# Performance work log

Measured on AMD Instinct MI355X. Metric: run time of the kernel, lower is better.

The kernel has to match this reference:

```python
import jax, jax.numpy as jnp
import numpy as np

FEATURE_DIM = 1024
N_HEADS = 16
D_K = 64
D_V = 64
B = 8
S = 1024
LN_EPS = 1e-5
NEG = 1e9


def setup_inputs() -> dict:
    key = jax.random.key(0)
    ks = jax.random.split(key, 7)
    sc = 0.02
    return {
        "input_Q": jax.random.normal(ks[0], (B, S, FEATURE_DIM), jnp.float32),
        "input_K": jax.random.normal(ks[1], (B, S, FEATURE_DIM), jnp.float32),
        "input_V": jax.random.normal(ks[2], (B, S, FEATURE_DIM), jnp.float32),
        "attn_mask": jnp.ones((B, S, S), jnp.float32),
        "W_Q": jax.random.normal(ks[3], (FEATURE_DIM, N_HEADS * D_K), jnp.float32) * sc,
        "W_K": jax.random.normal(ks[4], (FEATURE_DIM, N_HEADS * D_K), jnp.float32) * sc,
        "W_V": jax.random.normal(ks[5], (FEATURE_DIM, N_HEADS * D_V), jnp.float32) * sc,
        "W_O": jax.random.normal(ks[6], (N_HEADS * D_V, FEATURE_DIM), jnp.float32) * sc,
    }


def reference(input_Q, input_K, input_V, attn_mask, W_Q, W_K, W_V, W_O):
    b = input_Q.shape[0]
    # projections -> [b, h, s, d]
    Q = (input_Q @ W_Q).reshape(b, -1, N_HEADS, D_K).transpose(0, 2, 1, 3)
    K = (input_K @ W_K).reshape(b, -1, N_HEADS, D_K).transpose(0, 2, 1, 3)
    V = (input_V @ W_V).reshape(b, -1, N_HEADS, D_V).transpose(0, 2, 1, 3)
    # scores [b, h, sq, sk]
    scores = jnp.einsum("bhqd,bhkd->bhqk", Q, K) / np.sqrt(D_K).astype(np.float32)
    # additive mask: (mask - 1) * 1e9, broadcast over heads
    scores = scores + (attn_mask[:, None, :, :] - 1.0) * NEG
    attn = jax.nn.softmax(scores, axis=-1)
    # dropout is eval-mode identity (deterministic baseline)
    context = jnp.einsum("bhqk,bhkd->bhqd", attn, V)
    context = context.transpose(0, 2, 1, 3).reshape(b, -1, N_HEADS * D_V)
    output = context @ W_O
    x = output + input_Q  # residual
    # fresh nn.LayerNorm(feature_dim): weight=1, bias=0
    mu = jnp.mean(x, axis=-1, keepdims=True)
    var = jnp.var(x, axis=-1, keepdims=True)
    out = (x - mu) * jax.lax.rsqrt(var + LN_EPS)
    return out, attn
```

## Files before the change

kernel.cpp:

```cpp
#include <hip/hip_runtime.h>
#include <hip/hip_bf16.h>
#include <stdint.h>

typedef unsigned short u16;
typedef __attribute__((ext_vector_type(8))) short bf16x8;
typedef __attribute__((ext_vector_type(4))) float f32x4;

#define BATCH 8
#define SEQ   1024
#define FDIM  1024
#define NHEAD 16
#define DHEAD 64

__device__ __forceinline__ float bf2f(u16 u) {
  union { unsigned int i; float f; } v; v.i = ((unsigned int)u) << 16; return v.f;
}
__device__ __forceinline__ u16 f2bf(float f) {
  union { float f; unsigned int i; } v; v.f = f;
  unsigned int x = v.i;
  return (u16)((x + 0x7fffu + ((x >> 16) & 1u)) >> 16);
}

__device__ __forceinline__ uint4 load8(const u16* p) { return *(const uint4*)p; }
__device__ __forceinline__ uint4 load8(const float* p) {
  float4 a = *(const float4*)p;
  float4 b = *(const float4*)(p + 4);
  union { u16 h[8]; uint4 v; } r;
  r.h[0] = f2bf(a.x); r.h[1] = f2bf(a.y); r.h[2] = f2bf(a.z); r.h[3] = f2bf(a.w);
  r.h[4] = f2bf(b.x); r.h[5] = f2bf(b.y); r.h[6] = f2bf(b.z); r.h[7] = f2bf(b.w);
  return r.v;
}

__global__ __launch_bounds__(256) void transpose_k(
    const float* __restrict__ src, u16* __restrict__ dst, int srcLd, int dstLd) {
  __shared__ u16 t[64][72];
  const int r0 = blockIdx.y * 64, c0 = blockIdx.x * 64;
  const int tid = threadIdx.x;
  for (int p = 0; p < 16; ++p) {
    int idx = p * 256 + tid, r = idx >> 6, c = idx & 63;
    t[r][c] = f2bf(src[(long)(r0 + r) * srcLd + (c0 + c)]);
  }
  __syncthreads();
  for (int p = 0; p < 16; ++p) {
    int idx = p * 256 + tid, r = idx >> 6, c = idx & 63;
    dst[(long)(c0 + r) * dstLd + (r0 + c)] = t[c][r];
  }
}

template<int MODE, int WGM, int WGN, int MI, int NJ, typename AT>
__global__ __launch_bounds__(256) void gemm_bt(
    const AT* __restrict__ A, const u16* __restrict__ Bt, void* __restrict__ C,
    int K, int lda, int ldb, int ldc, long aZ, long bZ) {
  constexpr int BM = WGM * MI * 16;
  constexpr int BN = WGN * NJ * 16;
  __shared__ __align__(16) u16 As[BM][40];
  __shared__ __align__(16) u16 Bs[BN][40];
  const int tid = threadIdx.x;
  const int wave = tid >> 6, lane = tid & 63;
  const int quad = lane >> 4, l16 = lane & 15;
  const int wm = wave / WGN, wn = wave % WGN;
  const int m0 = blockIdx.y * BM, n0 = blockIdx.x * BN;
  const int z = blockIdx.z;
  A  += (long)z * aZ;
  Bt += (long)z * bZ;

  f32x4 acc[MI][NJ];
#pragma unroll
  for (int i = 0; i < MI; ++i)
#pragma unroll
    for (int j = 0; j < NJ; ++j) acc[i][j] = (f32x4){0.f, 0.f, 0.f, 0.f};

  const int srow = tid >> 2, scol = (tid & 3) * 8;
  for (int k0 = 0; k0 < K; k0 += 32) {
    __syncthreads();
#pragma unroll
    for (int p = 0; p < BM / 64; ++p) {
      int r = p * 64 + srow;
      *(uint4*)&As[r][scol] = load8(&A[(long)(m0 + r) * lda + k0 + scol]);
    }
#pragma unroll
    for (int p = 0; p < BN / 64; ++p) {
      int r = p * 64 + srow;
      *(uint4*)&Bs[r][scol] = load8(&Bt[(long)(n0 + r) * ldb + k0 + scol]);
    }
    __syncthreads();
    bf16x8 af[MI], bfr[NJ];
#pragma unroll
    for (int i = 0; i < MI; ++i)
      af[i] = *(const bf16x8*)&As[wm * MI * 16 + i * 16 + l16][quad * 8];
#pragma unroll
    for (int j = 0; j < NJ; ++j)
      bfr[j] = *(const bf16x8*)&Bs[wn * NJ * 16 + j * 16 + l16][quad * 8];
#pragma unroll
    for (int i = 0; i < MI; ++i)
#pragma unroll
      for (int j = 0; j < NJ; ++j)
        acc[i][j] = __builtin_amdgcn_mfma_f32_16x16x32_bf16(af[i], bfr[j], acc[i][j], 0, 0, 0);
  }

#pragma unroll
  for (int i = 0; i < MI; ++i) {
    const int rowb = m0 + wm * MI * 16 + i * 16 + quad * 4;
#pragma unroll
    for (int j = 0; j < NJ; ++j) {
      const int col = n0 + wn * NJ * 16 + j * 16 + l16;
#pragma unroll
      for (int r = 0; r < 4; ++r) {
        const float v = acc[i][j][r];
        const int row = rowb + r;
        if (MODE == 1) {
          ((float*)C)[(long)row * ldc + col] = v;
        } else if (MODE == 2) {
          int bb = row >> 10, ss = row & 1023, hh = col >> 6, dd = col & 63;
          ((u16*)C)[((long)(bb * NHEAD + hh) * SEQ + ss) * DHEAD + dd] = f2bf(v);
        } else if (MODE == 3) {
          int bb = row >> 10, ss = row & 1023, hh = col >> 6, dd = col & 63;
          ((u16*)C)[((long)(bb * NHEAD + hh) * DHEAD + dd) * SEQ + ss] = f2bf(v);
        } else {
          ((u16*)C)[(long)row * ldc + col] = f2bf(v);
        }
      }
    }
  }
}

__global__ __launch_bounds__(256, 4) void attn_kernel(
    const u16* __restrict__ Qb, const u16* __restrict__ Kb,
    const u16* __restrict__ Vt, const float* __restrict__ Msk,
    float* __restrict__ P, u16* __restrict__ Ctx) {
  __shared__ __align__(16) u16 QVs[64][72];
  __shared__ __align__(16) u16 Ks[64][72];
  __shared__ __align__(16) float Ps[64][68];
  const int tid = threadIdx.x, wave = tid >> 6, lane = tid & 63;
  const int quad = lane >> 4, l16 = lane & 15;
  const int q0 = blockIdx.x * 64, h = blockIdx.y, b = blockIdx.z;
  const long bh = (long)b * NHEAD + h;
  const u16* Qp = Qb + ((long)b * SEQ + q0) * FDIM + h * DHEAD;
  const u16* Kp = Kb + bh * SEQ * DHEAD;
  const u16* Vp = Vt + bh * (long)DHEAD * SEQ;
  const float* Mp = Msk + ((long)b * SEQ + q0) * SEQ;
  float* Pp = P + bh * (long)SEQ * SEQ + (long)q0 * SEQ;
  u16* Cp = Ctx + ((long)b * SEQ + q0) * FDIM + h * DHEAD;

  {
    int r = tid >> 3, c = (tid & 7) * 8;
    *(uint4*)&QVs[r][c]      = *(const uint4*)&Qp[(long)r * FDIM + c];
    *(uint4*)&QVs[r + 32][c] = *(const uint4*)&Qp[(long)(r + 32) * FDIM + c];
  }
  __syncthreads();
  const bf16x8 aq0 = *(const bf16x8*)&QVs[wave * 16 + l16][quad * 8];
  const bf16x8 aq1 = *(const bf16x8*)&QVs[wave * 16 + l16][32 + quad * 8];

  float m[4], l[4], rl[4];
#pragma unroll
  for (int r = 0; r < 4; ++r) { m[r] = -3.0e38f; l[r] = 0.f; }

  for (int st = 0; st < SEQ / 64; ++st) {
    const int sk0 = st * 64;
    __syncthreads();
    {
      int r = tid >> 3, c = (tid & 7) * 8;
      *(uint4*)&Ks[r][c]      = *(const uint4*)&Kp[(sk0 + r) * DHEAD + c];
      *(uint4*)&Ks[r + 32][c] = *(const uint4*)&Kp[(sk0 + r + 32) * DHEAD + c];
    }
    __syncthreads();
    float sv[4][4];
#pragma unroll
    for (int j = 0; j < 4; ++j) {
      bf16x8 bk0 = *(const bf16x8*)&Ks[j * 16 + l16][quad * 8];
      bf16x8 bk1 = *(const bf16x8*)&Ks[j * 16 + l16][32 + quad * 8];
      f32x4 sc = (f32x4){0.f, 0.f, 0.f, 0.f};
      sc = __builtin_amdgcn_mfma_f32_16x16x32_bf16(aq0, bk0, sc, 0, 0, 0);
      sc = __builtin_amdgcn_mfma_f32_16x16x32_bf16(aq1, bk1, sc, 0, 0, 0);
#pragma unroll
      for (int r = 0; r < 4; ++r) {
        int qr = wave * 16 + quad * 4 + r;
        float mk = Mp[(long)qr * SEQ + sk0 + j * 16 + l16];
        sv[j][r] = sc[r] * 0.125f + (mk - 1.0f) * 1.0e9f;
      }
    }
#pragma unroll
    for (int r = 0; r < 4; ++r) {
      float tm = fmaxf(fmaxf(sv[0][r], sv[1][r]), fmaxf(sv[2][r], sv[3][r]));
#pragma unroll
      for (int off = 1; off < 16; off <<= 1) tm = fmaxf(tm, __shfl_xor(tm, off, 64));
      float mn = fmaxf(m[r], tm);
      float ps = __expf(sv[0][r] - mn) + __expf(sv[1][r] - mn) +
                 __expf(sv[2][r] - mn) + __expf(sv[3][r] - mn);
#pragma unroll
      for (int off = 1; off < 16; off <<= 1) ps += __shfl_xor(ps, off, 64);
      l[r] = l[r] * __expf(m[r] - mn) + ps;
      m[r] = mn;
    }
  }
#pragma unroll
  for (int r = 0; r < 4; ++r) rl[r] = 1.0f / l[r];

  f32x4 acc[4];
#pragma unroll
  for (int n = 0; n < 4; ++n) acc[n] = (f32x4){0.f, 0.f, 0.f, 0.f};

  for (int st = 0; st < SEQ / 64; ++st) {
    const int sk0 = st * 64;
    __syncthreads();
    {
      int r = tid >> 3, c = (tid & 7) * 8;
      *(uint4*)&Ks[r][c]       = *(const uint4*)&Kp[(sk0 + r) * DHEAD + c];
      *(uint4*)&Ks[r + 32][c]  = *(const uint4*)&Kp[(sk0 + r + 32) * DHEAD + c];
      *(uint4*)&QVs[r][c]      = *(const uint4*)&Vp[(long)r * SEQ + sk0 + c];
      *(uint4*)&QVs[r + 32][c] = *(const uint4*)&Vp[(long)(r + 32) * SEQ + sk0 + c];
    }
    __syncthreads();
#pragma unroll
    for (int j = 0; j < 4; ++j) {
      bf16x8 bk0 = *(const bf16x8*)&Ks[j * 16 + l16][quad * 8];
      bf16x8 bk1 = *(const bf16x8*)&Ks[j * 16 + l16][32 + quad * 8];
      f32x4 sc = (f32x4){0.f, 0.f, 0.f, 0.f};
      sc = __builtin_amdgcn_mfma_f32_16x16x32_bf16(aq0, bk0, sc, 0, 0, 0);
      sc = __builtin_amdgcn_mfma_f32_16x16x32_bf16(aq1, bk1, sc, 0, 0, 0);
#pragma unroll
      for (int r = 0; r < 4; ++r) {
        int qr = wave * 16 + quad * 4 + r;
        float mk = Mp[(long)qr * SEQ + sk0 + j * 16 + l16];
        float s = sc[r] * 0.125f + (mk - 1.0f) * 1.0e9f;
        Ps[qr][j * 16 + l16] = __expf(s - m[r]) * rl[r];
      }
    }
    __syncthreads();
#pragma unroll
    for (int ks = 0; ks < 2; ++ks) {
      const float* pr = &Ps[wave * 16 + l16][ks * 32 + quad * 8];
      f32x4 plo = *(const f32x4*)pr;
      f32x4 phi = *(const f32x4*)(pr + 4);
      union { u16 h[8]; bf16x8 v; } pa;
      pa.h[0] = f2bf(plo.x); pa.h[1] = f2bf(plo.y);
      pa.h[2] = f2bf(plo.z); pa.h[3] = f2bf(plo.w);
      pa.h[4] = f2bf(phi.x); pa.h[5] = f2bf(phi.y);
      pa.h[6] = f2bf(phi.z); pa.h[7] = f2bf(phi.w);
#pragma unroll
      for (int n = 0; n < 4; ++n) {
        bf16x8 bv = *(const bf16x8*)&QVs[n * 16 + l16][ks * 32 + quad * 8];
        acc[n] = __builtin_amdgcn_mfma_f32_16x16x32_bf16(pa.v, bv, acc[n], 0, 0, 0);
      }
    }
#pragma unroll
    for (int rr = 0; rr < 4; ++rr) {
      const int row = wave * 16 + rr * 4 + quad;
      f32x4 val = *(const f32x4*)&Ps[row][l16 * 4];
      __builtin_nontemporal_store(val, (f32x4*)&Pp[(long)row * SEQ + sk0 + l16 * 4]);
    }
  }

#pragma unroll
  for (int n = 0; n < 4; ++n)
#pragma unroll
    for (int r = 0; r < 4; ++r)
      Cp[(long)(wave * 16 + quad * 4 + r) * FDIM + n * 16 + l16] = f2bf(acc[n][r]);
}

__global__ __launch_bounds__(256) void ln_kernel(
    const float* __restrict__ O, const float* __restrict__ Xq, float* __restrict__ out) {
  const int row = blockIdx.x, tid = threadIdx.x;
  const float4 o = *(const float4*)&O[(long)row * FDIM + tid * 4];
  const float4 q = *(const float4*)&Xq[(long)row * FDIM + tid * 4];
  float x[4] = { o.x + q.x, o.y + q.y, o.z + q.z, o.w + q.w };
  float s  = x[0] + x[1] + x[2] + x[3];
  float s2 = x[0]*x[0] + x[1]*x[1] + x[2]*x[2] + x[3]*x[3];
#pragma unroll
  for (int off = 32; off; off >>= 1) {
    s  += __shfl_xor(s, off, 64);
    s2 += __shfl_xor(s2, off, 64);
  }
  __shared__ float red[8];
  const int wave = tid >> 6, lane = tid & 63;
  if (lane == 0) { red[wave] = s; red[4 + wave] = s2; }
  __syncthreads();
  s  = red[0] + red[1] + red[2] + red[3];
  s2 = red[4] + red[5] + red[6] + red[7];
  const float mu = s * (1.0f / FDIM);
  const float var = s2 * (1.0f / FDIM) - mu * mu;
  const float rs = rsqrtf(var + 1e-5f);
  float4 res;
  res.x = (x[0] - mu) * rs; res.y = (x[1] - mu) * rs;
  res.z = (x[2] - mu) * rs; res.w = (x[3] - mu) * rs;
  *(float4*)&out[(long)row * FDIM + tid * 4] = res;
}

extern "C" void kernel_launch(void* const* d_in, const int* in_sizes, int n_in,
                              void* d_out, int out_size, void* d_ws, size_t ws_size,
                              hipStream_t stream) {
  const float* Xq = (const float*)d_in[0];
  const float* Xk = (const float*)d_in[1];
  const float* Xv = (const float*)d_in[2];
  const float* Mk = (const float*)d_in[3];
  const float* Wq = (const float*)d_in[4];
  const float* Wk = (const float*)d_in[5];
  const float* Wv = (const float*)d_in[6];
  const float* Wo = (const float*)d_in[7];

  u16* ws  = (u16*)d_ws;
  const size_t M = 1u << 20;
  u16* WtQ = ws;
  u16* WtK = ws + 1 * M;
  u16* WtV = ws + 2 * M;
  u16* WtO = ws + 3 * M;
  u16* Qb  = ws + 4 * M;
  u16* Kb  = ws + 12 * M;
  u16* Vt  = ws + 20 * M;
  float* O = (float*)(ws + 12 * M);

  float* out = (float*)d_out;
  float* P   = out + (size_t)BATCH * SEQ * FDIM;

  transpose_k<<<dim3(16, 16, 1), 256, 0, stream>>>(Wq, WtQ, FDIM, FDIM);
  transpose_k<<<dim3(16, 16, 1), 256, 0, stream>>>(Wk, WtK, FDIM, FDIM);
  transpose_k<<<dim3(16, 16, 1), 256, 0, stream>>>(Wv, WtV, FDIM, FDIM);
  transpose_k<<<dim3(16, 16, 1), 256, 0, stream>>>(Wo, WtO, FDIM, FDIM);
  gemm_bt<4, 2, 2, 4, 4><<<dim3(8, 64, 1), 256, 0, stream>>>(Xq, WtQ, Qb, FDIM, FDIM, FDIM, FDIM, 0, 0);
  gemm_bt<2, 2, 2, 4, 4><<<dim3(8, 64, 1), 256, 0, stream>>>(Xk, WtK, Kb, FDIM, FDIM, FDIM, 0, 0, 0);
  gemm_bt<3, 2, 2, 4, 4><<<dim3(8, 64, 1), 256, 0, stream>>>(Xv, WtV, Vt, FDIM, FDIM, FDIM, 0, 0, 0);
  attn_kernel<<<dim3(SEQ / 64, NHEAD, BATCH), 256, 0, stream>>>(Qb, Kb, Vt, Mk, P, Qb);
  gemm_bt<1, 2, 2, 4, 4><<<dim3(8, 64, 1), 256, 0, stream>>>(Qb, WtO, O, FDIM, FDIM, FDIM, FDIM, 0, 0);
  ln_kernel<<<dim3(BATCH * SEQ, 1, 1), 256, 0, stream>>>(O, Xq, out);
}
```

Before: 1.035 ms.

## Pre-convert inputs to bf16 and use direct global-to-LDS loads in GEMMs

```diff
diff --git a/kernel.cpp b/kernel.cpp
--- a/kernel.cpp
+++ b/kernel.cpp
@@ -3,6 +3,7 @@
 #include <stdint.h>
 
 typedef unsigned short u16;
+typedef unsigned int u32;
 typedef __attribute__((ext_vector_type(8))) short bf16x8;
 typedef __attribute__((ext_vector_type(4))) float f32x4;
 
@@ -31,6 +32,18 @@
   return r.v;
 }
 
+__device__ __forceinline__ void gload16(const u16* g, u16* l) {
+  __builtin_amdgcn_global_load_lds(
+      (__attribute__((address_space(1))) u32*)(u16*)g,
+      (__attribute__((address_space(3))) u32*)l, 16, 0, 0);
+}
+
+__global__ __launch_bounds__(256) void cvt_k(
+    const float* __restrict__ in, u16* __restrict__ out) {
+  const long i = ((long)blockIdx.x * 256 + threadIdx.x) * 8;
+  *(uint4*)&out[i] = load8(&in[i]);
+}
+
 __global__ __launch_bounds__(256) void transpose_k(
     const float* __restrict__ src, u16* __restrict__ dst, int srcLd, int dstLd) {
   __shared__ u16 t[64][72];
@@ -47,63 +60,62 @@
   }
 }
 
-template<int MODE, int WGM, int WGN, int MI, int NJ, typename AT>
-__global__ __launch_bounds__(256) void gemm_bt(
-    const AT* __restrict__ A, const u16* __restrict__ Bt, void* __restrict__ C,
-    int K, int lda, int ldb, int ldc, long aZ, long bZ) {
-  constexpr int BM = WGM * MI * 16;
-  constexpr int BN = WGN * NJ * 16;
-  __shared__ __align__(16) u16 As[BM][40];
-  __shared__ __align__(16) u16 Bs[BN][40];
+template<int MODE>
+__global__ __launch_bounds__(256) void gemm16(
+    const u16* __restrict__ A, const u16* __restrict__ Bt, void* __restrict__ C,
+    int K, int lda, int ldb, int ldc) {
+  __shared__ __align__(16) u16 As[128 * 32];
+  __shared__ __align__(16) u16 Bs[128 * 32];
   const int tid = threadIdx.x;
   const int wave = tid >> 6, lane = tid & 63;
   const int quad = lane >> 4, l16 = lane & 15;
-  const int wm = wave / WGN, wn = wave % WGN;
-  const int m0 = blockIdx.y * BM, n0 = blockIdx.x * BN;
-  const int z = blockIdx.z;
-  A  += (long)z * aZ;
-  Bt += (long)z * bZ;
-
-  f32x4 acc[MI][NJ];
-#pragma unroll
-  for (int i = 0; i < MI; ++i)
-#pragma unroll
-    for (int j = 0; j < NJ; ++j) acc[i][j] = (f32x4){0.f, 0.f, 0.f, 0.f};
-
-  const int srow = tid >> 2, scol = (tid & 3) * 8;
+  const int wm = wave >> 1, wn = wave & 1;
+  const int bid = blockIdx.y * 8 + blockIdx.x;
+  const int cpx = (gridDim.y * 8) >> 3;
+  const int swz = (bid & 7) * cpx + (bid >> 3);
+  const int m0 = (swz >> 3) * 128, n0 = (swz & 7) * 128;
+
+  f32x4 acc[4][4];
+#pragma unroll
+  for (int i = 0; i < 4; ++i)
+#pragma unroll
+    for (int j = 0; j < 4; ++j) acc[i][j] = (f32x4){0.f, 0.f, 0.f, 0.f};
+
+  const int srow = lane >> 2, scol = (lane & 3) * 8;
+  const u16* ga = &A[(long)(m0 + wave * 32 + srow) * lda + scol];
+  const u16* gb = &Bt[(long)(n0 + wave * 32 + srow) * ldb + scol];
+  u16* la0 = &As[(wave * 32) * 32];
+  u16* la1 = &As[(wave * 32 + 16) * 32];
+  u16* lb0 = &Bs[(wave * 32) * 32];
+  u16* lb1 = &Bs[(wave * 32 + 16) * 32];
+
   for (int k0 = 0; k0 < K; k0 += 32) {
     __syncthreads();
-#pragma unroll
-    for (int p = 0; p < BM / 64; ++p) {
-      int r = p * 64 + srow;
-      *(uint4*)&As[r][scol] = load8(&A[(long)(m0 + r) * lda + k0 + scol]);
-    }
-#pragma unroll
-    for (int p = 0; p < BN / 64; ++p) {
-      int r = p * 64 + srow;
-      *(uint4*)&Bs[r][scol] = load8(&Bt[(long)(n0 + r) * ldb + k0 + scol]);
-    }
-    __syncthreads();
-    bf16x8 af[MI], bfr[NJ];
-#pragma unroll
-    for (int i = 0; i < MI; ++i)
-      af[i] = *(const bf16x8*)&As[wm * MI * 16 + i * 16 + l16][quad * 8];
-#pragma unroll
-    for (int j = 0; j < NJ; ++j)
-      bfr[j] = *(const bf16x8*)&Bs[wn * NJ * 16 + j * 16 + l16][quad * 8];
-#pragma unroll
-    for (int i = 0; i < MI; ++i)
-#pragma unroll
-      for (int j = 0; j < NJ; ++j)
+    gload16(ga + k0,            la0);
+    gload16(ga + k0 + 16 * lda, la1);
+    gload16(gb + k0,            lb0);
+    gload16(gb + k0 + 16 * ldb, lb1);
+    __syncthreads();
+    bf16x8 af[4], bfr[4];
+#pragma unroll
+    for (int i = 0; i < 4; ++i)
+      af[i] = *(const bf16x8*)&As[(wm * 64 + i * 16 + l16) * 32 + quad * 8];
+#pragma unroll
+    for (int j = 0; j < 4; ++j)
+      bfr[j] = *(const bf16x8*)&Bs[(wn * 64 + j * 16 + l16) * 32 + quad * 8];
+#pragma unroll
+    for (int i = 0; i < 4; ++i)
+#pragma unroll
+      for (int j = 0; j < 4; ++j)
         acc[i][j] = __builtin_amdgcn_mfma_f32_16x16x32_bf16(af[i], bfr[j], acc[i][j], 0, 0, 0);
   }
 
 #pragma unroll
-  for (int i = 0; i < MI; ++i) {
-    const int rowb = m0 + wm * MI * 16 + i * 16 + quad * 4;
-#pragma unroll
-    for (int j = 0; j < NJ; ++j) {
-      const int col = n0 + wn * NJ * 16 + j * 16 + l16;
+  for (int i = 0; i < 4; ++i) {
+    const int rowb = m0 + wm * 64 + i * 16 + quad * 4;
+#pragma unroll
+    for (int j = 0; j < 4; ++j) {
+      const int col = n0 + wn * 64 + j * 16 + l16;
 #pragma unroll
       for (int r = 0; r < 4; ++r) {
         const float v = acc[i][j][r];
@@ -312,14 +324,21 @@
   float* out = (float*)d_out;
   float* P   = out + (size_t)BATCH * SEQ * FDIM;
 
+  u16* Xqb = (u16*)P;
+  u16* Xkb = (u16*)P + 8 * M;
+  u16* Xvb = (u16*)P + 16 * M;
+
+  cvt_k<<<dim3(4096, 1, 1), 256, 0, stream>>>(Xq, Xqb);
+  cvt_k<<<dim3(4096, 1, 1), 256, 0, stream>>>(Xk, Xkb);
+  cvt_k<<<dim3(4096, 1, 1), 256, 0, stream>>>(Xv, Xvb);
   transpose_k<<<dim3(16, 16, 1), 256, 0, stream>>>(Wq, WtQ, FDIM, FDIM);
   transpose_k<<<dim3(16, 16, 1), 256, 0, stream>>>(Wk, WtK, FDIM, FDIM);
   transpose_k<<<dim3(16, 16, 1), 256, 0, stream>>>(Wv, WtV, FDIM, FDIM);
   transpose_k<<<dim3(16, 16, 1), 256, 0, stream>>>(Wo, WtO, FDIM, FDIM);
-  gemm_bt<4, 2, 2, 4, 4><<<dim3(8, 64, 1), 256, 0, stream>>>(Xq, WtQ, Qb, FDIM, FDIM, FDIM, FDIM, 0, 0);
-  gemm_bt<2, 2, 2, 4, 4><<<dim3(8, 64, 1), 256, 0, stream>>>(Xk, WtK, Kb, FDIM, FDIM, FDIM, 0, 0, 0);
-  gemm_bt<3, 2, 2, 4, 4><<<dim3(8, 64, 1), 256, 0, stream>>>(Xv, WtV, Vt, FDIM, FDIM, FDIM, 0, 0, 0);
+  gemm16<4><<<dim3(8, 64, 1), 256, 0, stream>>>(Xqb, WtQ, Qb, FDIM, FDIM, FDIM, FDIM);
+  gemm16<2><<<dim3(8, 64, 1), 256, 0, stream>>>(Xkb, WtK, Kb, FDIM, FDIM, FDIM, 0);
+  gemm16<3><<<dim3(8, 64, 1), 256, 0, stream>>>(Xvb, WtV, Vt, FDIM, FDIM, FDIM, 0);
   attn_kernel<<<dim3(SEQ / 64, NHEAD, BATCH), 256, 0, stream>>>(Qb, Kb, Vt, Mk, P, Qb);
-  gemm_bt<1, 2, 2, 4, 4><<<dim3(8, 64, 1), 256, 0, stream>>>(Qb, WtO, O, FDIM, FDIM, FDIM, FDIM, 0, 0);
+  gemm16<1><<<dim3(8, 64, 1), 256, 0, stream>>>(Qb, WtO, O, FDIM, FDIM, FDIM, FDIM);
   ln_kernel<<<dim3(BATCH * SEQ, 1, 1), 256, 0, stream>>>(O, Xq, out);
 }
```

Result: faster. 1.004 ms (-3.0%).
